# Kernel tuning notes

Measured on AMD Instinct MI355X. Metric: run time of the kernel, lower is better.

Reference implementation:

```python
import jax, jax.numpy as jnp
import numpy as np

NP, NQ = 8192, 8192
DP, DQ = 512, 512
D1, D2 = 256, 256
DEG = 32  # avg degree for synthetic bipartite adjacency


def setup_inputs() -> dict:
    key = jax.random.key(0)
    ks = list(jax.random.split(key, 40))
    it = iter(ks)

    def nk():
        return next(it)

    hp = jax.random.normal(nk(), (NP, DP), jnp.float32)
    hq = jax.random.normal(nk(), (NQ, DQ), jnp.float32)

    def adj(shape):
        # sparse-ish binary adjacency, ~DEG neighbors per row
        return (jax.random.uniform(nk(), shape) < DEG / shape[1]).astype(jnp.float32)

    a_cons = adj((NP, NQ))
    a_prod = adj((NQ, NP))
    a_rev_cons = adj((NQ, NP))
    a_rev_prod = adj((NP, NQ))

    def lin(din, dout):
        s = (6.0 / (din + dout)) ** 0.5  # xavier_uniform, gain=1
        w = jax.random.uniform(nk(), (dout, din), jnp.float32, minval=-s, maxval=s)
        return w, jnp.zeros((dout,), jnp.float32)

    d = dict(hp=hp, hq=hq, a_cons=a_cons, a_prod=a_prod,
             a_rev_cons=a_rev_cons, a_rev_prod=a_rev_prod)
    d['wp1_w'], d['wp1_b'] = lin(DP, D1)
    d['wq1_w'], d['wq1_b'] = lin(DQ, D1)
    d['wcons1_w'], d['wcons1_b'] = lin(DQ, D1)
    d['wrprod1_w'], d['wrprod1_b'] = lin(DQ, D1)
    d['wprod1_w'], d['wprod1_b'] = lin(DP, D1)
    d['wrcons1_w'], d['wrcons1_b'] = lin(DP, D1)
    d['wp2_w'], d['wp2_b'] = lin(D1, D2)
    d['wq2_w'], d['wq2_b'] = lin(D1, D2)
    d['wcons2_w'], d['wcons2_b'] = lin(D1, D2)
    d['wrprod2_w'], d['wrprod2_b'] = lin(D1, D2)
    d['wprod2_w'], d['wprod2_b'] = lin(D1, D2)
    d['wrcons2_w'], d['wrcons2_b'] = lin(D1, D2)
    return d


def reference(hp, hq, a_cons, a_prod, a_rev_cons, a_rev_prod,
              wp1_w, wp1_b, wq1_w, wq1_b, wcons1_w, wcons1_b,
              wrprod1_w, wrprod1_b, wprod1_w, wprod1_b, wrcons1_w, wrcons1_b,
              wp2_w, wp2_b, wq2_w, wq2_b, wcons2_w, wcons2_b,
              wrprod2_w, wrprod2_b, wprod2_w, wprod2_b, wrcons2_w, wrcons2_b):
    lin = lambda x, w, b: x @ w.T + b
    act = lambda x: jax.nn.leaky_relu(x, 0.1)
    # layer 1 (dropout is identity in eval mode)
    hp1 = act(lin(hp, wp1_w, wp1_b)
              + a_cons @ lin(hq, wcons1_w, wcons1_b)
              + a_rev_prod @ lin(hq, wrprod1_w, wrprod1_b))
    hq1 = act(lin(hq, wq1_w, wq1_b)
              + a_prod @ lin(hp, wprod1_w, wprod1_b)
              + a_rev_cons @ lin(hp, wrcons1_w, wrcons1_b))
    # layer 2
    hp2 = act(lin(hp1, wp2_w, wp2_b)
              + a_cons @ lin(hq1, wcons2_w, wcons2_b)
              + a_rev_prod @ lin(hq1, wrprod2_w, wrprod2_b))
    hq2 = act(lin(hq1, wq2_w, wq2_b)
              + a_prod @ lin(hp1, wprod2_w, wprod2_b)
              + a_rev_cons @ lin(hp1, wrcons2_w, wrcons2_b))
    norm = lambda x: x / (jnp.linalg.norm(x, axis=1, keepdims=True) + 1e-9)
    return norm(hp2), norm(hq2)
```

## Files before the change

### kernel.cpp

```cpp
#include <hip/hip_runtime.h>

#define CAP 128

typedef __attribute__((ext_vector_type(8))) short bf16x8;
typedef __attribute__((ext_vector_type(4))) float f32x4;
typedef __attribute__((ext_vector_type(4))) float f32x4v;

__device__ __forceinline__ unsigned short f2bf(float f) {
    unsigned u = __float_as_uint(f);
    u += 0x7FFFu + ((u >> 16) & 1u);
    return (unsigned short)(u >> 16);
}
__device__ __forceinline__ float bf2f(unsigned short h) {
    return __uint_as_float(((unsigned)h) << 16);
}

struct CvtSeg { const float* s; unsigned short* d; int n4; };
struct CvtArgs { CvtSeg seg[14]; };

__global__ __launch_bounds__(256) void cvt_kernel(CvtArgs c) {
    int gid = blockIdx.x * 256 + threadIdx.x;
    int stride = gridDim.x * 256;
    #pragma unroll
    for (int si = 0; si < 14; ++si) {
        CvtSeg sg = c.seg[si];
        for (int i = gid; i < sg.n4; i += stride) {
            float4 v = ((const float4*)sg.s)[i];
            ushort4 o;
            o.x = f2bf(v.x); o.y = f2bf(v.y); o.z = f2bf(v.z); o.w = f2bf(v.w);
            ((ushort4*)sg.d)[i] = o;
        }
    }
}

struct ExtArgs { const float* a0; const float* a1; const float* a2; const float* a3; int* idx; int* cnt; };

__device__ __forceinline__ void extract_body(const ExtArgs& e, int row, int m) {
    int t = threadIdx.x;
    int wave = t >> 6, lane = t & 63;
    const float* A = (m == 0) ? e.a0 : (m == 1) ? e.a1 : (m == 2) ? e.a2 : e.a3;
    const f32x4v* rp = (const f32x4v*)(A + (size_t)row * 8192);
    unsigned mask = 0;
    #pragma unroll
    for (int it = 0; it < 8; ++it) {
        f32x4v v = __builtin_nontemporal_load(&rp[it * 256 + t]);
        mask |= (unsigned)(v.x != 0.f) << (4 * it);
        mask |= (unsigned)(v.y != 0.f) << (4 * it + 1);
        mask |= (unsigned)(v.z != 0.f) << (4 * it + 2);
        mask |= (unsigned)(v.w != 0.f) << (4 * it + 3);
    }
    int cnt = __popc(mask);
    int pre = cnt;
    #pragma unroll
    for (int off = 1; off < 64; off <<= 1) {
        int u = __shfl_up(pre, off);
        if (lane >= off) pre += u;
    }
    __shared__ int lwt[4];
    if (lane == 63) lwt[wave] = pre;
    __syncthreads();
    int wbase = 0;
    if (wave > 0) wbase += lwt[0];
    if (wave > 1) wbase += lwt[1];
    if (wave > 2) wbase += lwt[2];
    int o = wbase + pre - cnt;
    int* op = e.idx + ((size_t)m * 8192 + row) * CAP;
    while (mask) {
        int b = __ffs((int)mask) - 1;
        mask &= mask - 1;
        int j = (b >> 2) * 1024 + t * 4 + (b & 3);
        if (o < CAP) op[o] = j;
        o++;
    }
    if (t == 0) {
        int tot = lwt[0] + lwt[1] + lwt[2] + lwt[3];
        e.cnt[m * 8192 + row] = tot < CAP ? tot : CAP;
    }
}

struct GemmDesc { const unsigned short* X; const unsigned short* W; const float* bias; unsigned short* Z; };
struct GemmArgs { GemmDesc d[6]; };

template<int K>
__device__ __forceinline__ void gemm_slim_body(const GemmArgs& ga, int bx, int by, int bz) {
    GemmDesc g = ga.d[bz];
    int wave = threadIdx.x >> 6;
    int lane = threadIdx.x & 63;
    int r = lane & 15, q = lane >> 4;
    int rowbase = bx * 128 + wave * 32;
    int colbase = by * 32;
    f32x4 acc[2][2] = {};
    const unsigned short* xp0 = g.X + (size_t)(rowbase + r) * K + q * 8;
    const unsigned short* xp1 = xp0 + (size_t)16 * K;
    const unsigned short* wb0 = g.W + (size_t)(colbase + r) * K + q * 8;
    const unsigned short* wb1 = wb0 + (size_t)16 * K;
    #pragma unroll 4
    for (int k0 = 0; k0 < K; k0 += 32) {
        bf16x8 a0 = *(const bf16x8*)(xp0 + k0);
        bf16x8 a1 = *(const bf16x8*)(xp1 + k0);
        bf16x8 b0 = *(const bf16x8*)(wb0 + k0);
        bf16x8 b1 = *(const bf16x8*)(wb1 + k0);
        acc[0][0] = __builtin_amdgcn_mfma_f32_16x16x32_bf16(a0, b0, acc[0][0], 0, 0, 0);
        acc[0][1] = __builtin_amdgcn_mfma_f32_16x16x32_bf16(a0, b1, acc[0][1], 0, 0, 0);
        acc[1][0] = __builtin_amdgcn_mfma_f32_16x16x32_bf16(a1, b0, acc[1][0], 0, 0, 0);
        acc[1][1] = __builtin_amdgcn_mfma_f32_16x16x32_bf16(a1, b1, acc[1][1], 0, 0, 0);
    }
    #pragma unroll
    for (int mt = 0; mt < 2; ++mt) {
        #pragma unroll
        for (int nt = 0; nt < 2; ++nt) {
            int col = colbase + nt * 16 + r;
            float bv = g.bias[col];
            #pragma unroll
            for (int j = 0; j < 4; ++j) {
                int row = rowbase + mt * 16 + q * 4 + j;
                g.Z[(size_t)row * 256 + col] = f2bf(acc[mt][nt][j] + bv);
            }
        }
    }
}

__global__ __launch_bounds__(256, 8) void fused_ext_gemm_kernel(ExtArgs e, GemmArgs ga) {
    int bid = blockIdx.x;
    int gemmIdx = -1, extIdx;
    if (bid < 27648) {
        int grp = bid / 9, rem = bid % 9;
        if (rem == 0) gemmIdx = grp;
        extIdx = grp * 8 + (rem - 1);
    } else {
        extIdx = 24576 + (bid - 27648);
    }
    if (gemmIdx >= 0) {
        gemm_slim_body<512>(ga, gemmIdx & 63, (gemmIdx >> 6) & 7, gemmIdx >> 9);
    } else {
        extract_body(e, extIdx & 8191, extIdx >> 13);
    }
}

template<int K>
__global__ __launch_bounds__(256) void gemm6_kernel(GemmArgs ga) {
    GemmDesc g = ga.d[blockIdx.z];
    int wave = threadIdx.x >> 6;
    int lane = threadIdx.x & 63;
    int r = lane & 15, q = lane >> 4;
    int rowbase = blockIdx.x * 128 + wave * 32;
    int colbase = blockIdx.y * 64;
    f32x4 acc[2][4] = {};
    const unsigned short* xp0 = g.X + (size_t)(rowbase + r) * K + q * 8;
    const unsigned short* xp1 = xp0 + (size_t)16 * K;
    const unsigned short* wbase = g.W + (size_t)(colbase + r) * K + q * 8;
    #pragma unroll
    for (int k0 = 0; k0 < K; k0 += 32) {
        bf16x8 a0 = *(const bf16x8*)(xp0 + k0);
        bf16x8 a1 = *(const bf16x8*)(xp1 + k0);
        #pragma unroll
        for (int nt = 0; nt < 4; ++nt) {
            bf16x8 b = *(const bf16x8*)(wbase + (size_t)nt * 16 * K + k0);
            acc[0][nt] = __builtin_amdgcn_mfma_f32_16x16x32_bf16(a0, b, acc[0][nt], 0, 0, 0);
            acc[1][nt] = __builtin_amdgcn_mfma_f32_16x16x32_bf16(a1, b, acc[1][nt], 0, 0, 0);
        }
    }
    #pragma unroll
    for (int mt = 0; mt < 2; ++mt) {
        #pragma unroll
        for (int nt = 0; nt < 4; ++nt) {
            int col = colbase + nt * 16 + r;
            float bv = g.bias[col];
            #pragma unroll
            for (int j = 0; j < 4; ++j) {
                int row = rowbase + mt * 16 + q * 4 + j;
                g.Z[(size_t)row * 256 + col] = f2bf(acc[mt][nt][j] + bv);
            }
        }
    }
}

struct AggSide {
    const unsigned short* zself;
    const unsigned short* za;
    const unsigned short* zb;
    const int* idxa; const int* cnta;
    const int* idxb; const int* cntb;
    unsigned short* out_bf;
    float* out_f;
};

template<int FINAL>
__global__ __launch_bounds__(256) void agg_kernel(AggSide s0, AggSide s1) {
    AggSide s = blockIdx.y ? s1 : s0;
    int t = threadIdx.x;
    int l32 = t & 31;
    int row = blockIdx.x * 8 + (t >> 5);
    int c8 = l32 * 8;
    bf16x8 v = *(const bf16x8*)(s.zself + (size_t)row * 256 + c8);
    float acc[8];
    #pragma unroll
    for (int j = 0; j < 8; ++j) acc[j] = bf2f((unsigned short)v[j]);
    int ca = s.cnta[row], cb = s.cntb[row];
    const int* ia = s.idxa + (size_t)row * CAP;
    const int* ib = s.idxb + (size_t)row * CAP;
    #pragma unroll 4
    for (int k = 0; k < ca; ++k) {
        int na = ia[k];
        bf16x8 w = *(const bf16x8*)(s.za + (size_t)na * 256 + c8);
        #pragma unroll
        for (int j = 0; j < 8; ++j) acc[j] += bf2f((unsigned short)w[j]);
    }
    #pragma unroll 4
    for (int k = 0; k < cb; ++k) {
        int nb = ib[k];
        bf16x8 w = *(const bf16x8*)(s.zb + (size_t)nb * 256 + c8);
        #pragma unroll
        for (int j = 0; j < 8; ++j) acc[j] += bf2f((unsigned short)w[j]);
    }
    #pragma unroll
    for (int j = 0; j < 8; ++j) acc[j] = acc[j] > 0.f ? acc[j] : 0.1f * acc[j];
    if (FINAL) {
        float ss = 0.f;
        #pragma unroll
        for (int j = 0; j < 8; ++j) ss += acc[j] * acc[j];
        #pragma unroll
        for (int off = 1; off < 32; off <<= 1) ss += __shfl_xor(ss, off);
        float sc = 1.0f / (sqrtf(ss) + 1e-9f);
        float4 o0, o1;
        o0.x = acc[0] * sc; o0.y = acc[1] * sc; o0.z = acc[2] * sc; o0.w = acc[3] * sc;
        o1.x = acc[4] * sc; o1.y = acc[5] * sc; o1.z = acc[6] * sc; o1.w = acc[7] * sc;
        float* op = s.out_f + (size_t)row * 256 + c8;
        *(float4*)op = o0;
        *(float4*)(op + 4) = o1;
    } else {
        bf16x8 o;
        #pragma unroll
        for (int j = 0; j < 8; ++j) o[j] = (short)f2bf(acc[j]);
        *(bf16x8*)(s.out_bf + (size_t)row * 256 + c8) = o;
    }
}

extern "C" void kernel_launch(void* const* d_in, const int* in_sizes, int n_in,
                              void* d_out, int out_size, void* d_ws, size_t ws_size,
                              hipStream_t stream) {
    const float* hp         = (const float*)d_in[0];
    const float* hq         = (const float*)d_in[1];
    const float* a_cons     = (const float*)d_in[2];
    const float* a_prod     = (const float*)d_in[3];
    const float* a_rev_cons = (const float*)d_in[4];
    const float* a_rev_prod = (const float*)d_in[5];

    char* ws = (char*)d_ws;
    constexpr size_t SZ_H   = (size_t)8192 * 512 * 2;
    constexpr size_t SZ_W1  = (size_t)256 * 512 * 2;
    constexpr size_t SZ_W2  = (size_t)256 * 256 * 2;
    constexpr size_t SZ_Z   = (size_t)8192 * 256 * 2;
    constexpr size_t OFF_HP  = 0;
    constexpr size_t OFF_HQ  = OFF_HP + SZ_H;
    constexpr size_t OFF_WBF = OFF_HQ + SZ_H;
    constexpr size_t OFF_IDX = OFF_WBF + 6 * SZ_W1 + 6 * SZ_W2;
    constexpr size_t OFF_CNT = OFF_IDX + (size_t)4 * 8192 * CAP * 4;
    constexpr size_t OFF_Z   = OFF_CNT + (size_t)4 * 8192 * 4;
    constexpr size_t OFF_H1P = OFF_Z + 6 * SZ_Z;
    constexpr size_t OFF_H1Q = OFF_H1P + SZ_Z;

    unsigned short* hp_bf = (unsigned short*)(ws + OFF_HP);
    unsigned short* hq_bf = (unsigned short*)(ws + OFF_HQ);
    int* idx = (int*)(ws + OFF_IDX);
    int* cnt = (int*)(ws + OFF_CNT);
    unsigned short* z[6];
    for (int i = 0; i < 6; ++i) z[i] = (unsigned short*)(ws + OFF_Z + i * SZ_Z);
    unsigned short* h1p = (unsigned short*)(ws + OFF_H1P);
    unsigned short* h1q = (unsigned short*)(ws + OFF_H1Q);

    unsigned short* wbf[12];
    for (int i = 0; i < 6; ++i) wbf[i]     = (unsigned short*)(ws + OFF_WBF + i * SZ_W1);
    for (int i = 0; i < 6; ++i) wbf[6 + i] = (unsigned short*)(ws + OFF_WBF + 6 * SZ_W1 + i * SZ_W2);

    CvtArgs ca;
    ca.seg[0] = { hp, hp_bf, 8192 * 512 / 4 };
    ca.seg[1] = { hq, hq_bf, 8192 * 512 / 4 };
    const int wIdxL1[6] = { 6, 10, 12, 8, 14, 16 };
    const int wIdxL2[6] = { 18, 22, 24, 20, 26, 28 };
    for (int i = 0; i < 6; ++i) ca.seg[2 + i] = { (const float*)d_in[wIdxL1[i]], wbf[i],     256 * 512 / 4 };
    for (int i = 0; i < 6; ++i) ca.seg[8 + i] = { (const float*)d_in[wIdxL2[i]], wbf[6 + i], 256 * 256 / 4 };
    cvt_kernel<<<dim3(1024), dim3(256), 0, stream>>>(ca);

    ExtArgs ea = { a_cons, a_prod, a_rev_cons, a_rev_prod, idx, cnt };
    GemmArgs g1;
    g1.d[0] = { hp_bf, wbf[0], (const float*)d_in[7],  z[0] };
    g1.d[1] = { hq_bf, wbf[1], (const float*)d_in[11], z[1] };
    g1.d[2] = { hq_bf, wbf[2], (const float*)d_in[13], z[2] };
    g1.d[3] = { hq_bf, wbf[3], (const float*)d_in[9],  z[3] };
    g1.d[4] = { hp_bf, wbf[4], (const float*)d_in[15], z[4] };
    g1.d[5] = { hp_bf, wbf[5], (const float*)d_in[17], z[5] };
    fused_ext_gemm_kernel<<<dim3(35840), dim3(256), 0, stream>>>(ea, g1);

    int* idx0 = idx + (size_t)0 * 8192 * CAP;
    int* idx1 = idx + (size_t)1 * 8192 * CAP;
    int* idx2 = idx + (size_t)2 * 8192 * CAP;
    int* idx3 = idx + (size_t)3 * 8192 * CAP;
    int* cnt0 = cnt, *cnt1 = cnt + 8192, *cnt2 = cnt + 16384, *cnt3 = cnt + 24576;

    AggSide p1 = { z[0], z[1], z[2], idx0, cnt0, idx3, cnt3, h1p, nullptr };
    AggSide q1 = { z[3], z[4], z[5], idx1, cnt1, idx2, cnt2, h1q, nullptr };
    agg_kernel<0><<<dim3(1024, 2), dim3(256), 0, stream>>>(p1, q1);

    GemmArgs g2;
    g2.d[0] = { h1p, wbf[6],  (const float*)d_in[19], z[0] };
    g2.d[1] = { h1q, wbf[7],  (const float*)d_in[23], z[1] };
    g2.d[2] = { h1q, wbf[8],  (const float*)d_in[25], z[2] };
    g2.d[3] = { h1q, wbf[9],  (const float*)d_in[21], z[3] };
    g2.d[4] = { h1p, wbf[10], (const float*)d_in[27], z[4] };
    g2.d[5] = { h1p, wbf[11], (const float*)d_in[29], z[5] };
    gemm6_kernel<256><<<dim3(64, 4, 6), dim3(256), 0, stream>>>(g2);

    float* outp = (float*)d_out;
    AggSide p2 = { z[0], z[1], z[2], idx0, cnt0, idx3, cnt3, nullptr, outp };
    AggSide q2 = { z[3], z[4], z[5], idx1, cnt1, idx2, cnt2, nullptr, outp + (size_t)8192 * 256 };
    agg_kernel<1><<<dim3(1024, 2), dim3(256), 0, stream>>>(p2, q2);
}
```

Baseline: 370.3 us.

## Split aggregation into 64-column panels for cache locality, add separate norm pass

The aggregation kernel now assigns each block 32 rows by one 64-column panel, with 8 lanes per row, instead of 8 full 256-column rows. Consecutive blocks share a chunk and cover the four panels of both sides, so each wave gathers a narrower slice of the Z tables, which may give better cache hit rates on the random neighbor gathers. Because a row's squared norm is now spread across four blocks, the final pass writes per-panel partial sums and a new norm_kernel rescales the output. This costs an extra launch plus a read and write of the output, and each gather now moves only 128 bytes per row, giving less memory-level parallelism per neighbor.

```diff
diff --git a/kernel.cpp b/kernel.cpp
--- a/kernel.cpp
+++ b/kernel.cpp
@@ -186,13 +186,17 @@
 };
 
 template<int FINAL>
-__global__ __launch_bounds__(256) void agg_kernel(AggSide s0, AggSide s1) {
-    AggSide s = blockIdx.y ? s1 : s0;
+__global__ __launch_bounds__(256) void agg_kernel(AggSide s0, AggSide s1, float* partial) {
+    int bid = blockIdx.x;
+    int side = (bid >> 2) & 1;
+    int panel = bid & 3;
+    int chunk = bid >> 3;
+    AggSide s = side ? s1 : s0;
     int t = threadIdx.x;
-    int l32 = t & 31;
-    int row = blockIdx.x * 8 + (t >> 5);
-    int c8 = l32 * 8;
-    bf16x8 v = *(const bf16x8*)(s.zself + (size_t)row * 256 + c8);
+    int unit = t >> 3, l8 = t & 7;
+    int row = chunk * 32 + unit;
+    int col = panel * 64 + l8 * 8;
+    bf16x8 v = *(const bf16x8*)(s.zself + (size_t)row * 256 + col);
     float acc[8];
     #pragma unroll
     for (int j = 0; j < 8; ++j) acc[j] = bf2f((unsigned short)v[j]);
@@ -202,14 +206,14 @@
     #pragma unroll 4
     for (int k = 0; k < ca; ++k) {
         int na = ia[k];
-        bf16x8 w = *(const bf16x8*)(s.za + (size_t)na * 256 + c8);
+        bf16x8 w = *(const bf16x8*)(s.za + (size_t)na * 256 + col);
         #pragma unroll
         for (int j = 0; j < 8; ++j) acc[j] += bf2f((unsigned short)w[j]);
     }
     #pragma unroll 4
     for (int k = 0; k < cb; ++k) {
         int nb = ib[k];
-        bf16x8 w = *(const bf16x8*)(s.zb + (size_t)nb * 256 + c8);
+        bf16x8 w = *(const bf16x8*)(s.zb + (size_t)nb * 256 + col);
         #pragma unroll
         for (int j = 0; j < 8; ++j) acc[j] += bf2f((unsigned short)w[j]);
     }
@@ -220,19 +224,35 @@
         #pragma unroll
         for (int j = 0; j < 8; ++j) ss += acc[j] * acc[j];
         #pragma unroll
-        for (int off = 1; off < 32; off <<= 1) ss += __shfl_xor(ss, off);
-        float sc = 1.0f / (sqrtf(ss) + 1e-9f);
+        for (int off = 1; off < 8; off <<= 1) ss += __shfl_xor(ss, off);
+        float* op = s.out_f + (size_t)row * 256 + col;
         float4 o0, o1;
-        o0.x = acc[0] * sc; o0.y = acc[1] * sc; o0.z = acc[2] * sc; o0.w = acc[3] * sc;
-        o1.x = acc[4] * sc; o1.y = acc[5] * sc; o1.z = acc[6] * sc; o1.w = acc[7] * sc;
-        float* op = s.out_f + (size_t)row * 256 + c8;
+        o0.x = acc[0]; o0.y = acc[1]; o0.z = acc[2]; o0.w = acc[3];
+        o1.x = acc[4]; o1.y = acc[5]; o1.z = acc[6]; o1.w = acc[7];
         *(float4*)op = o0;
         *(float4*)(op + 4) = o1;
+        if (l8 == 0) partial[((size_t)(side * 8192 + row)) * 4 + panel] = ss;
     } else {
         bf16x8 o;
         #pragma unroll
         for (int j = 0; j < 8; ++j) o[j] = (short)f2bf(acc[j]);
-        *(bf16x8*)(s.out_bf + (size_t)row * 256 + c8) = o;
+        *(bf16x8*)(s.out_bf + (size_t)row * 256 + col) = o;
+    }
+}
+
+__global__ __launch_bounds__(256) void norm_kernel(float* out, const float* partial) {
+    int t = threadIdx.x;
+    int unit = t >> 3, l8 = t & 7;
+    int row = blockIdx.x * 32 + unit;
+    const float* pp = partial + (size_t)row * 4;
+    float ss = pp[0] + pp[1] + pp[2] + pp[3];
+    float sc = 1.0f / (sqrtf(ss) + 1e-9f);
+    float4* rp = (float4*)(out + (size_t)row * 256) + l8 * 8;
+    #pragma unroll
+    for (int j = 0; j < 8; ++j) {
+        float4 v = rp[j];
+        v.x *= sc; v.y *= sc; v.z *= sc; v.w *= sc;
+        rp[j] = v;
     }
 }
 
@@ -259,6 +279,7 @@
     constexpr size_t OFF_Z   = OFF_CNT + (size_t)4 * 8192 * 4;
     constexpr size_t OFF_H1P = OFF_Z + 6 * SZ_Z;
     constexpr size_t OFF_H1Q = OFF_H1P + SZ_Z;
+    constexpr size_t OFF_PART = OFF_H1Q + SZ_Z;
 
     unsigned short* hp_bf = (unsigned short*)(ws + OFF_HP);
     unsigned short* hq_bf = (unsigned short*)(ws + OFF_HQ);
@@ -268,6 +289,7 @@
     for (int i = 0; i < 6; ++i) z[i] = (unsigned short*)(ws + OFF_Z + i * SZ_Z);
     unsigned short* h1p = (unsigned short*)(ws + OFF_H1P);
     unsigned short* h1q = (unsigned short*)(ws + OFF_H1Q);
+    float* partial = (float*)(ws + OFF_PART);
 
     unsigned short* wbf[12];
     for (int i = 0; i < 6; ++i) wbf[i]     = (unsigned short*)(ws + OFF_WBF + i * SZ_W1);
@@ -300,7 +322,7 @@
 
     AggSide p1 = { z[0], z[1], z[2], idx0, cnt0, idx3, cnt3, h1p, nullptr };
     AggSide q1 = { z[3], z[4], z[5], idx1, cnt1, idx2, cnt2, h1q, nullptr };
-    agg_kernel<0><<<dim3(1024, 2), dim3(256), 0, stream>>>(p1, q1);
+    agg_kernel<0><<<dim3(2048), dim3(256), 0, stream>>>(p1, q1, nullptr);
 
     GemmArgs g2;
     g2.d[0] = { h1p, wbf[6],  (const float*)d_in[19], z[0] };
@@ -314,5 +336,6 @@
     float* outp = (float*)d_out;
     AggSide p2 = { z[0], z[1], z[2], idx0, cnt0, idx3, cnt3, nullptr, outp };
     AggSide q2 = { z[3], z[4], z[5], idx1, cnt1, idx2, cnt2, nullptr, outp + (size_t)8192 * 256 };
-    agg_kernel<1><<<dim3(1024, 2), dim3(256), 0, stream>>>(p2, q2);
-}
+    agg_kernel<1><<<dim3(2048), dim3(256), 0, stream>>>(p2, q2, partial);
+    norm_kernel<<<dim3(512), dim3(256), 0, stream>>>(outp, partial);
+}
```

Result: no change. 374.5 us (+1.1%).
